# Kernel optimization log

Measured on AMD Instinct MI355X. Metric: run time of the kernel, lower is better.

Reference implementation:

```python
import jax, jax.numpy as jnp
import numpy as np

SIGMA = 1.0

def _pairwise_sqdist(x, y):
    # x: [N,3], y: [M,3] -> [N,M] squared distances via gram expansion
    xx = jnp.sum(x * x, axis=-1)[:, None]
    yy = jnp.sum(y * y, axis=-1)[None, :]
    xy = x @ y.T
    return jnp.maximum(xx + yy - 2.0 * xy, 0.0)

def _cauchy(d2, sigma):
    return 1.0 / (1.0 + d2 / (sigma * sigma))

def setup_inputs() -> dict:
    key = jax.random.key(0)
    k1, k2, k3, k4 = jax.random.split(key, 4)
    V, N, M = 4096, 8192, 8192
    src_vertices = jax.random.normal(k1, (V, 3), dtype=jnp.float32)
    tar_normals = jax.random.normal(k2, (M, 3), dtype=jnp.float32)
    tar_centers = jax.random.normal(k3, (M, 3), dtype=jnp.float32)
    src_indices = jax.random.randint(k4, (N, 3), 0, V)
    return {"src_vertices": src_vertices, "tar_normals": tar_normals,
            "tar_centers": tar_centers, "src_indices": src_indices}

def reference(src_vertices, tar_normals, tar_centers, src_indices):
    # Gather triangle vertices: [N,3(verts),3(xyz)]
    tris = src_vertices[src_indices]
    a, b, c = tris[:, 0, :], tris[:, 1, :], tris[:, 2, :]
    normals = 0.5 * jnp.cross(a - b, c - b)        # [N,3]
    centers = tris.sum(axis=1) / 3.0               # [N,3]

    # Currents energy with cauchy kernel K(x,y) = 1/(1 + |x-y|^2/sigma^2)
    K_ss = _cauchy(_pairwise_sqdist(centers, centers), SIGMA)      # [N,N]
    K_st = _cauchy(_pairwise_sqdist(centers, tar_centers), SIGMA)  # [N,M]
    K_tt = _cauchy(_pairwise_sqdist(tar_centers, tar_centers), SIGMA)  # [M,M]

    e_ss = jnp.sum(K_ss * (normals @ normals.T))
    e_st = jnp.sum(K_st * (normals @ tar_normals.T))
    e_tt = jnp.sum(K_tt * (tar_normals @ tar_normals.T))
    return e_ss - 2.0 * e_st + e_tt
```

## Files before the change

### kernel.cpp

```cpp
#include <hip/hip_runtime.h>

typedef short bf16x8 __attribute__((ext_vector_type(8)));
typedef float f32x16 __attribute__((ext_vector_type(16)));

static __device__ __forceinline__ unsigned short f2bf(float x) {
    unsigned u = __builtin_bit_cast(unsigned, x);
    unsigned r = (u + 0x7FFFu + ((u >> 16) & 1u)) >> 16;
    return (unsigned short)r;
}
static __device__ __forceinline__ float bf2f(unsigned short h) {
    unsigned u = (unsigned)h << 16;
    return __builtin_bit_cast(float, u);
}

__global__ void dc_pack(const float* __restrict__ verts,
                        const float* __restrict__ tnorm,
                        const float* __restrict__ tcent,
                        const int* __restrict__ idx,
                        unsigned short* __restrict__ ws,
                        float* __restrict__ out,
                        int N, int M) {
    int p = blockIdx.x * blockDim.x + threadIdx.x;
    if (p == 0) out[0] = 0.0f;
    int P = N + M;
    if (p >= P) return;

    float cx, cy, cz, nx, ny, nz;
    if (p < N) {
        int i0 = idx[3 * p + 0], i1 = idx[3 * p + 1], i2 = idx[3 * p + 2];
        float ax = verts[3 * i0], ay = verts[3 * i0 + 1], az = verts[3 * i0 + 2];
        float bx = verts[3 * i1], by = verts[3 * i1 + 1], bz = verts[3 * i1 + 2];
        float qx = verts[3 * i2], qy = verts[3 * i2 + 1], qz = verts[3 * i2 + 2];
        float ux = ax - bx, uy = ay - by, uz = az - bz;
        float vx = qx - bx, vy = qy - by, vz = qz - bz;
        nx = 0.5f * (uy * vz - uz * vy);
        ny = 0.5f * (uz * vx - ux * vz);
        nz = 0.5f * (ux * vy - uy * vx);
        cx = (ax + bx + qx) * (1.0f / 3.0f);
        cy = (ay + by + qy) * (1.0f / 3.0f);
        cz = (az + bz + qz) * (1.0f / 3.0f);
    } else {
        int t = p - N;
        cx = tcent[3 * t]; cy = tcent[3 * t + 1]; cz = tcent[3 * t + 2];
        nx = -tnorm[3 * t]; ny = -tnorm[3 * t + 1]; nz = -tnorm[3 * t + 2];
    }

    unsigned short chx = f2bf(cx), chy = f2bf(cy), chz = f2bf(cz);
    unsigned short clx = f2bf(cx - bf2f(chx));
    unsigned short cly = f2bf(cy - bf2f(chy));
    unsigned short clz = f2bf(cz - bf2f(chz));
    unsigned short nhx = f2bf(nx), nhy = f2bf(ny), nhz = f2bf(nz);
    unsigned short nlx = f2bf(nx - bf2f(nhx));
    unsigned short nly = f2bf(ny - bf2f(nhy));
    unsigned short nlz = f2bf(nz - bf2f(nhz));
    float ex = bf2f(chx) + bf2f(clx);
    float ey = bf2f(chy) + bf2f(cly);
    float ez = bf2f(chz) + bf2f(clz);
    float s = ex * ex + ey * ey + ez * ez;
    unsigned short sh = f2bf(s), sl = f2bf(s - bf2f(sh));
    unsigned short m2hx = f2bf(-2.0f * bf2f(chx)), m2hy = f2bf(-2.0f * bf2f(chy)), m2hz = f2bf(-2.0f * bf2f(chz));
    unsigned short m2lx = f2bf(-2.0f * bf2f(clx)), m2ly = f2bf(-2.0f * bf2f(cly)), m2lz = f2bf(-2.0f * bf2f(clz));
    const unsigned short one = 0x3F80;

    __align__(16) unsigned short A1v[16] = {
        m2hx, m2hy, m2hz,  m2hx, m2hy, m2hz,  m2lx, m2ly, m2lz,
        sh, sl,  one, one,  one,  0, 0 };
    __align__(16) unsigned short B1v[16] = {
        chx, chy, chz,  clx, cly, clz,  chx, chy, chz,
        one, one,  sh, sl,  one,  0, 0 };
    __align__(16) unsigned short A2v[16] = {
        nhx, nhy, nhz,  nhx, nhy, nhz,  nlx, nly, nlz,
        0, 0, 0, 0, 0, 0, 0 };
    __align__(16) unsigned short B2v[16] = {
        nhx, nhy, nhz,  nlx, nly, nlz,  nhx, nhy, nhz,
        0, 0, 0, 0, 0, 0, 0 };

    size_t arr = (size_t)P * 16;
    unsigned short* A1 = ws;
    unsigned short* B1 = ws + arr;
    unsigned short* A2 = ws + 2 * arr;
    unsigned short* B2 = ws + 3 * arr;

    int tile = p >> 5, m = p & 31;
    size_t lo = ((size_t)tile * 64 + m) * 8;
    size_t hi = lo + 32 * 8;

    *(uint4*)(A1 + lo) = *(const uint4*)&A1v[0];
    *(uint4*)(A1 + hi) = *(const uint4*)&A1v[8];
    *(uint4*)(B1 + lo) = *(const uint4*)&B1v[0];
    *(uint4*)(B1 + hi) = *(const uint4*)&B1v[8];
    *(uint4*)(A2 + lo) = *(const uint4*)&A2v[0];
    *(uint4*)(A2 + hi) = *(const uint4*)&A2v[8];
    *(uint4*)(B2 + lo) = *(const uint4*)&B2v[0];
    *(uint4*)(B2 + hi) = *(const uint4*)&B2v[8];
}

template <bool HALF>
static __device__ __forceinline__ void acc4(float4& part, const f32x16& d1, const f32x16& d2) {
#pragma unroll
    for (int g = 0; g < 4; ++g) {
        const int r = 4 * g;
        float p01 = d1[r] * d1[r + 1];
        float p23 = d1[r + 2] * d1[r + 3];
        float n01 = fmaf(d2[r], d1[r + 1], d2[r + 1] * d1[r]);
        float n23 = fmaf(d2[r + 2], d1[r + 3], d2[r + 3] * d1[r + 2]);
        float t   = p01 * p23;
        float num = fmaf(n01, p23, n23 * p01);
        float rk  = __builtin_amdgcn_rcpf(t);
        if (HALF) rk *= 0.5f;
        (&part.x)[g] = fmaf(num, rk, (&part.x)[g]);
    }
}

__global__ __launch_bounds__(256, 5) void dc_pair_mfma(
    const unsigned short* __restrict__ ws, float* __restrict__ out, int P) {
    __shared__ float wsum[4];

    const int nT = P >> 5;
    const int half = nT >> 1;
    size_t arr = (size_t)P * 16;
    const unsigned short* A1 = ws;
    const unsigned short* B1 = ws + arr;
    const unsigned short* A2 = ws + 2 * arr;
    const unsigned short* B2 = ws + 3 * arr;

    int tid = threadIdx.x;
    int lane = tid & 63, wv = tid >> 6;
    int g = blockIdx.x * 4 + wv;
    int I = g / 10;
    int c = g - 10 * I;

    int st  = c * 26 - (c > 7 ? c - 7 : 0);
    int len = 26 - (c >= 7 ? 1 : 0);

    bf16x8 a1 = *(const bf16x8*)(A1 + ((size_t)I * 64 + lane) * 8);
    bf16x8 a2 = *(const bf16x8*)(A2 + ((size_t)I * 64 + lane) * 8);

    const f32x16 zero = {0.f,0.f,0.f,0.f,0.f,0.f,0.f,0.f,0.f,0.f,0.f,0.f,0.f,0.f,0.f,0.f};
    float4 part = make_float4(0.f, 0.f, 0.f, 0.f);

#pragma unroll 2
    for (int it = 0; it < len; ++it) {
        int d = st + it;
        int j = I + d;
        int jm = (j >= nT) ? j - nT : j;
        const bf16x8 b1 = *(const bf16x8*)(B1 + ((size_t)jm * 64 + lane) * 8);
        const bf16x8 b2 = *(const bf16x8*)(B2 + ((size_t)jm * 64 + lane) * 8);
        f32x16 d1 = __builtin_amdgcn_mfma_f32_32x32x16_bf16(a1, b1, zero, 0, 0, 0);
        f32x16 d2 = __builtin_amdgcn_mfma_f32_32x32x16_bf16(a2, b2, zero, 0, 0, 0);
        if (d == 0 || d == half) acc4<true>(part, d1, d2);
        else                     acc4<false>(part, d1, d2);
    }

    float s = (part.x + part.y + part.z + part.w) * 2.0f;
#pragma unroll
    for (int off = 32; off > 0; off >>= 1) s += __shfl_down(s, off, 64);
    if (lane == 0) wsum[wv] = s;
    __syncthreads();
    if (tid == 0) {
        float t = wsum[0] + wsum[1] + wsum[2] + wsum[3];
        atomicAdd(out, t);
    }
}

extern "C" void kernel_launch(void* const* d_in, const int* in_sizes, int n_in,
                              void* d_out, int out_size, void* d_ws, size_t ws_size,
                              hipStream_t stream) {
    const float* verts = (const float*)d_in[0];
    const float* tnorm = (const float*)d_in[1];
    const float* tcent = (const float*)d_in[2];
    const int*   sidx  = (const int*)d_in[3];

    int M = in_sizes[1] / 3;
    int N = in_sizes[3] / 3;
    int P = N + M;

    unsigned short* ws = (unsigned short*)d_ws;
    float* out = (float*)d_out;

    int bblocks = (P + 255) / 256;
    dc_pack<<<bblocks, 256, 0, stream>>>(verts, tnorm, tcent, sidx, ws, out, N, M);

    int nT = P >> 5;
    int nBlocks = (nT * 10) / 4;
    dc_pair_mfma<<<nBlocks, 256, 0, stream>>>(ws, out, P);
}
```

Before: 90.42 us.

## Interleave B operands, prefetch next tile, and peel diagonal and half-diagonal tiles

Result: faster. 87.54 us (-3.2%).

```diff
diff --git a/kernel.cpp b/kernel.cpp
--- a/kernel.cpp
+++ b/kernel.cpp
@@ -12,6 +12,7 @@
     unsigned u = (unsigned)h << 16;
     return __builtin_bit_cast(float, u);
 }
+
 
 __global__ void dc_pack(const float* __restrict__ verts,
                         const float* __restrict__ tnorm,
@@ -77,9 +78,8 @@
 
     size_t arr = (size_t)P * 16;
     unsigned short* A1 = ws;
-    unsigned short* B1 = ws + arr;
-    unsigned short* A2 = ws + 2 * arr;
-    unsigned short* B2 = ws + 3 * arr;
+    unsigned short* A2 = ws + arr;
+    unsigned short* BB = ws + 2 * arr;
 
     int tile = p >> 5, m = p & 31;
     size_t lo = ((size_t)tile * 64 + m) * 8;
@@ -87,15 +87,17 @@
 
     *(uint4*)(A1 + lo) = *(const uint4*)&A1v[0];
     *(uint4*)(A1 + hi) = *(const uint4*)&A1v[8];
-    *(uint4*)(B1 + lo) = *(const uint4*)&B1v[0];
-    *(uint4*)(B1 + hi) = *(const uint4*)&B1v[8];
     *(uint4*)(A2 + lo) = *(const uint4*)&A2v[0];
     *(uint4*)(A2 + hi) = *(const uint4*)&A2v[8];
-    *(uint4*)(B2 + lo) = *(const uint4*)&B2v[0];
-    *(uint4*)(B2 + hi) = *(const uint4*)&B2v[8];
-}
-
-template <bool HALF>
+
+    size_t blo = ((size_t)tile * 64 + m) * 16;
+    size_t bhi = ((size_t)tile * 64 + 32 + m) * 16;
+    *(uint4*)(BB + blo)     = *(const uint4*)&B1v[0];
+    *(uint4*)(BB + blo + 8) = *(const uint4*)&B2v[0];
+    *(uint4*)(BB + bhi)     = *(const uint4*)&B1v[8];
+    *(uint4*)(BB + bhi + 8) = *(const uint4*)&B2v[8];
+}
+
 static __device__ __forceinline__ void acc4(float4& part, const f32x16& d1, const f32x16& d2) {
 #pragma unroll
     for (int g = 0; g < 4; ++g) {
@@ -106,9 +108,7 @@
         float n23 = fmaf(d2[r + 2], d1[r + 3], d2[r + 3] * d1[r + 2]);
         float t   = p01 * p23;
         float num = fmaf(n01, p23, n23 * p01);
-        float rk  = __builtin_amdgcn_rcpf(t);
-        if (HALF) rk *= 0.5f;
-        (&part.x)[g] = fmaf(num, rk, (&part.x)[g]);
+        (&part.x)[g] = fmaf(num, __builtin_amdgcn_rcpf(t), (&part.x)[g]);
     }
 }
 
@@ -117,12 +117,10 @@
     __shared__ float wsum[4];
 
     const int nT = P >> 5;
-    const int half = nT >> 1;
     size_t arr = (size_t)P * 16;
     const unsigned short* A1 = ws;
-    const unsigned short* B1 = ws + arr;
-    const unsigned short* A2 = ws + 2 * arr;
-    const unsigned short* B2 = ws + 3 * arr;
+    const unsigned short* A2 = ws + arr;
+    const unsigned short* BB = ws + 2 * arr;
 
     int tid = threadIdx.x;
     int lane = tid & 63, wv = tid >> 6;
@@ -132,27 +130,66 @@
 
     int st  = c * 26 - (c > 7 ? c - 7 : 0);
     int len = 26 - (c >= 7 ? 1 : 0);
+    int d0 = st, L = len, extra = 0, extraTile = 0;
+    if (c == 0) { d0 = 1; L = 25; extra = 1; extraTile = I; }
+    else if (c == 9) { L = 24; extra = 1;
+        extraTile = I + 256 - ((I + 256 >= nT) ? nT : 0); }
 
     bf16x8 a1 = *(const bf16x8*)(A1 + ((size_t)I * 64 + lane) * 8);
     bf16x8 a2 = *(const bf16x8*)(A2 + ((size_t)I * 64 + lane) * 8);
 
     const f32x16 zero = {0.f,0.f,0.f,0.f,0.f,0.f,0.f,0.f,0.f,0.f,0.f,0.f,0.f,0.f,0.f,0.f};
-    float4 part = make_float4(0.f, 0.f, 0.f, 0.f);
-
+    float4 partA = make_float4(0.f, 0.f, 0.f, 0.f);
+    float4 partB = make_float4(0.f, 0.f, 0.f, 0.f);
+
+    int js   = I + d0;
+    int len1 = nT - js; if (len1 > L) len1 = L; if (len1 < 0) len1 = 0;
+    int len2 = L - len1;
+    int startA = (len1 > 0) ? js : js - nT;
+
+    const size_t laneOff = (size_t)lane * 16;
+
+    {
+        const unsigned short* pb = BB + (size_t)startA * 1024 + laneOff;
+        bf16x8 b1 = *(const bf16x8*)pb;
+        bf16x8 b2 = *(const bf16x8*)(pb + 8);
 #pragma unroll 2
-    for (int it = 0; it < len; ++it) {
-        int d = st + it;
-        int j = I + d;
-        int jm = (j >= nT) ? j - nT : j;
-        const bf16x8 b1 = *(const bf16x8*)(B1 + ((size_t)jm * 64 + lane) * 8);
-        const bf16x8 b2 = *(const bf16x8*)(B2 + ((size_t)jm * 64 + lane) * 8);
+        for (int it = 0; it < len1; ++it) {
+            pb += 1024;
+            bf16x8 nb1 = *(const bf16x8*)pb;
+            bf16x8 nb2 = *(const bf16x8*)(pb + 8);
+            f32x16 d1 = __builtin_amdgcn_mfma_f32_32x32x16_bf16(a1, b1, zero, 0, 0, 0);
+            f32x16 d2 = __builtin_amdgcn_mfma_f32_32x32x16_bf16(a2, b2, zero, 0, 0, 0);
+            acc4(partA, d1, d2);
+            b1 = nb1; b2 = nb2;
+        }
+    }
+    if (len2 > 0) {
+        const unsigned short* pb = BB + (size_t)(js + len1 - nT) * 1024 + laneOff;
+        bf16x8 b1 = *(const bf16x8*)pb;
+        bf16x8 b2 = *(const bf16x8*)(pb + 8);
+#pragma unroll 2
+        for (int it = 0; it < len2; ++it) {
+            pb += 1024;
+            bf16x8 nb1 = *(const bf16x8*)pb;
+            bf16x8 nb2 = *(const bf16x8*)(pb + 8);
+            f32x16 d1 = __builtin_amdgcn_mfma_f32_32x32x16_bf16(a1, b1, zero, 0, 0, 0);
+            f32x16 d2 = __builtin_amdgcn_mfma_f32_32x32x16_bf16(a2, b2, zero, 0, 0, 0);
+            acc4(partA, d1, d2);
+            b1 = nb1; b2 = nb2;
+        }
+    }
+    for (int e = 0; e < extra; ++e) {
+        const unsigned short* pb = BB + (size_t)extraTile * 1024 + laneOff;
+        bf16x8 b1 = *(const bf16x8*)pb;
+        bf16x8 b2 = *(const bf16x8*)(pb + 8);
         f32x16 d1 = __builtin_amdgcn_mfma_f32_32x32x16_bf16(a1, b1, zero, 0, 0, 0);
         f32x16 d2 = __builtin_amdgcn_mfma_f32_32x32x16_bf16(a2, b2, zero, 0, 0, 0);
-        if (d == 0 || d == half) acc4<true>(part, d1, d2);
-        else                     acc4<false>(part, d1, d2);
-    }
-
-    float s = (part.x + part.y + part.z + part.w) * 2.0f;
+        acc4(partB, d1, d2);
+    }
+
+    float s = 2.0f * (partA.x + partA.y + partA.z + partA.w)
+            + (partB.x + partB.y + partB.z + partB.w);
 #pragma unroll
     for (int off = 32; off > 0; off >>= 1) s += __shfl_down(s, off, 64);
     if (lane == 0) wsum[wv] = s;
```

## Process two row tiles per wave to reuse B loads, software-prefetch B

Applied to the files above, without the earlier changes.

New measurement: 83.75 us. -7.4%, faster.

```diff
diff --git a/kernel.cpp b/kernel.cpp
--- a/kernel.cpp
+++ b/kernel.cpp
@@ -12,6 +12,7 @@
     unsigned u = (unsigned)h << 16;
     return __builtin_bit_cast(float, u);
 }
+
 
 __global__ void dc_pack(const float* __restrict__ verts,
                         const float* __restrict__ tnorm,
@@ -77,8 +78,8 @@
 
     size_t arr = (size_t)P * 16;
     unsigned short* A1 = ws;
-    unsigned short* B1 = ws + arr;
-    unsigned short* A2 = ws + 2 * arr;
+    unsigned short* A2 = ws + arr;
+    unsigned short* B1 = ws + 2 * arr;
     unsigned short* B2 = ws + 3 * arr;
 
     int tile = p >> 5, m = p & 31;
@@ -87,15 +88,14 @@
 
     *(uint4*)(A1 + lo) = *(const uint4*)&A1v[0];
     *(uint4*)(A1 + hi) = *(const uint4*)&A1v[8];
+    *(uint4*)(A2 + lo) = *(const uint4*)&A2v[0];
+    *(uint4*)(A2 + hi) = *(const uint4*)&A2v[8];
     *(uint4*)(B1 + lo) = *(const uint4*)&B1v[0];
     *(uint4*)(B1 + hi) = *(const uint4*)&B1v[8];
-    *(uint4*)(A2 + lo) = *(const uint4*)&A2v[0];
-    *(uint4*)(A2 + hi) = *(const uint4*)&A2v[8];
     *(uint4*)(B2 + lo) = *(const uint4*)&B2v[0];
     *(uint4*)(B2 + hi) = *(const uint4*)&B2v[8];
 }
 
-template <bool HALF>
 static __device__ __forceinline__ void acc4(float4& part, const f32x16& d1, const f32x16& d2) {
 #pragma unroll
     for (int g = 0; g < 4; ++g) {
@@ -106,53 +106,84 @@
         float n23 = fmaf(d2[r + 2], d1[r + 3], d2[r + 3] * d1[r + 2]);
         float t   = p01 * p23;
         float num = fmaf(n01, p23, n23 * p01);
-        float rk  = __builtin_amdgcn_rcpf(t);
-        if (HALF) rk *= 0.5f;
-        (&part.x)[g] = fmaf(num, rk, (&part.x)[g]);
-    }
-}
-
-__global__ __launch_bounds__(256, 5) void dc_pair_mfma(
+        (&part.x)[g] = fmaf(num, __builtin_amdgcn_rcpf(t), (&part.x)[g]);
+    }
+}
+
+__global__ __launch_bounds__(256, 4) void dc_pair_mfma(
     const unsigned short* __restrict__ ws, float* __restrict__ out, int P) {
     __shared__ float wsum[4];
 
     const int nT = P >> 5;
-    const int half = nT >> 1;
     size_t arr = (size_t)P * 16;
     const unsigned short* A1 = ws;
-    const unsigned short* B1 = ws + arr;
-    const unsigned short* A2 = ws + 2 * arr;
+    const unsigned short* A2 = ws + arr;
+    const unsigned short* B1 = ws + 2 * arr;
     const unsigned short* B2 = ws + 3 * arr;
 
     int tid = threadIdx.x;
     int lane = tid & 63, wv = tid >> 6;
-    int g = blockIdx.x * 4 + wv;
-    int I = g / 10;
-    int c = g - 10 * I;
-
-    int st  = c * 26 - (c > 7 ? c - 7 : 0);
-    int len = 26 - (c >= 7 ? 1 : 0);
-
-    bf16x8 a1 = *(const bf16x8*)(A1 + ((size_t)I * 64 + lane) * 8);
-    bf16x8 a2 = *(const bf16x8*)(A2 + ((size_t)I * 64 + lane) * 8);
+    int gi = blockIdx.x * 4 + wv;
+    int rp = gi >> 4, c = gi & 15;
+    int I0 = 2 * rp, I1 = I0 + 1;
+
+    const size_t lo = (size_t)lane * 8;
+
+    bf16x8 a1_0 = *(const bf16x8*)(A1 + (size_t)I0 * 512 + lo);
+    bf16x8 a2_0 = *(const bf16x8*)(A2 + (size_t)I0 * 512 + lo);
+    bf16x8 a1_1 = *(const bf16x8*)(A1 + (size_t)I1 * 512 + lo);
+    bf16x8 a2_1 = *(const bf16x8*)(A2 + (size_t)I1 * 512 + lo);
 
     const f32x16 zero = {0.f,0.f,0.f,0.f,0.f,0.f,0.f,0.f,0.f,0.f,0.f,0.f,0.f,0.f,0.f,0.f};
-    float4 part = make_float4(0.f, 0.f, 0.f, 0.f);
-
-#pragma unroll 2
-    for (int it = 0; it < len; ++it) {
-        int d = st + it;
-        int j = I + d;
-        int jm = (j >= nT) ? j - nT : j;
-        const bf16x8 b1 = *(const bf16x8*)(B1 + ((size_t)jm * 64 + lane) * 8);
-        const bf16x8 b2 = *(const bf16x8*)(B2 + ((size_t)jm * 64 + lane) * 8);
-        f32x16 d1 = __builtin_amdgcn_mfma_f32_32x32x16_bf16(a1, b1, zero, 0, 0, 0);
-        f32x16 d2 = __builtin_amdgcn_mfma_f32_32x32x16_bf16(a2, b2, zero, 0, 0, 0);
-        if (d == 0 || d == half) acc4<true>(part, d1, d2);
-        else                     acc4<false>(part, d1, d2);
-    }
-
-    float s = (part.x + part.y + part.z + part.w) * 2.0f;
+    float4 partA = make_float4(0.f, 0.f, 0.f, 0.f);
+    float4 corrP = make_float4(0.f, 0.f, 0.f, 0.f);
+    float4 corrM = make_float4(0.f, 0.f, 0.f, 0.f);
+
+    auto run = [&](int startTile, int n) {
+        const unsigned short* p1 = B1 + (size_t)startTile * 512 + lo;
+        const unsigned short* p2 = B2 + (size_t)startTile * 512 + lo;
+        bf16x8 b1 = *(const bf16x8*)p1;
+        bf16x8 b2 = *(const bf16x8*)p2;
+        for (int it = 0; it < n; ++it) {
+            p1 += 512; p2 += 512;
+            bf16x8 nb1 = *(const bf16x8*)p1;
+            bf16x8 nb2 = *(const bf16x8*)p2;
+            f32x16 d1 = __builtin_amdgcn_mfma_f32_32x32x16_bf16(a1_0, b1, zero, 0, 0, 0);
+            f32x16 d2 = __builtin_amdgcn_mfma_f32_32x32x16_bf16(a2_0, b2, zero, 0, 0, 0);
+            acc4(partA, d1, d2);
+            d1 = __builtin_amdgcn_mfma_f32_32x32x16_bf16(a1_1, b1, zero, 0, 0, 0);
+            d2 = __builtin_amdgcn_mfma_f32_32x32x16_bf16(a2_1, b2, zero, 0, 0, 0);
+            acc4(partA, d1, d2);
+            b1 = nb1; b2 = nb2;
+        }
+    };
+    auto one_tile = [&](float4& part, const bf16x8& x1, const bf16x8& x2, int jm) {
+        const bf16x8 b1 = *(const bf16x8*)(B1 + (size_t)jm * 512 + lo);
+        const bf16x8 b2 = *(const bf16x8*)(B2 + (size_t)jm * 512 + lo);
+        f32x16 d1 = __builtin_amdgcn_mfma_f32_32x32x16_bf16(x1, b1, zero, 0, 0, 0);
+        f32x16 d2 = __builtin_amdgcn_mfma_f32_32x32x16_bf16(x2, b2, zero, 0, 0, 0);
+        acc4(part, d1, d2);
+    };
+
+    int js = I0 + 1 + 16 * c;
+    int len1 = nT - js; if (len1 > 16) len1 = 16; if (len1 < 0) len1 = 0;
+    int len2 = 16 - len1;
+    if (len1 > 0) run(js, len1);
+    if (len2 > 0) run(js + len1 - nT, len2);
+
+    if (c == 0) {
+        one_tile(corrP, a1_0, a2_0, I0);
+        one_tile(corrM, a1_1, a2_1, I0 + 1);
+    } else if (c == 15) {
+        int v = I0 + 256; if (v >= nT) v -= nT;
+        int y = I0 + 257; if (y >= nT) y -= nT;
+        one_tile(corrM, a1_0, a2_0, v);
+        one_tile(corrP, a1_1, a2_1, y);
+    }
+
+    float s = 2.0f * (partA.x + partA.y + partA.z + partA.w)
+            + (corrP.x + corrP.y + corrP.z + corrP.w)
+            - (corrM.x + corrM.y + corrM.z + corrM.w);
 #pragma unroll
     for (int off = 32; off > 0; off >>= 1) s += __shfl_down(s, off, 64);
     if (lane == 0) wsum[wv] = s;
@@ -181,7 +212,5 @@
     int bblocks = (P + 255) / 256;
     dc_pack<<<bblocks, 256, 0, stream>>>(verts, tnorm, tcent, sidx, ws, out, N, M);
 
-    int nT = P >> 5;
-    int nBlocks = (nT * 10) / 4;
-    dc_pair_mfma<<<nBlocks, 256, 0, stream>>>(ws, out, P);
-}
+    dc_pair_mfma<<<1024, 256, 0, stream>>>(ws, out, P);
+}
```

## Re-partition the pair-tile loop into fixed 16-tile chunks with diagonal corrections

Applied to the files above, without the earlier changes.

After: 95.94 us. 1.06x slower.

```diff
diff --git a/kernel.cpp b/kernel.cpp
--- a/kernel.cpp
+++ b/kernel.cpp
@@ -12,6 +12,7 @@
     unsigned u = (unsigned)h << 16;
     return __builtin_bit_cast(float, u);
 }
+
 
 __global__ void dc_pack(const float* __restrict__ verts,
                         const float* __restrict__ tnorm,
@@ -77,8 +78,8 @@
 
     size_t arr = (size_t)P * 16;
     unsigned short* A1 = ws;
-    unsigned short* B1 = ws + arr;
-    unsigned short* A2 = ws + 2 * arr;
+    unsigned short* A2 = ws + arr;
+    unsigned short* B1 = ws + 2 * arr;
     unsigned short* B2 = ws + 3 * arr;
 
     int tile = p >> 5, m = p & 31;
@@ -87,15 +88,14 @@
 
     *(uint4*)(A1 + lo) = *(const uint4*)&A1v[0];
     *(uint4*)(A1 + hi) = *(const uint4*)&A1v[8];
+    *(uint4*)(A2 + lo) = *(const uint4*)&A2v[0];
+    *(uint4*)(A2 + hi) = *(const uint4*)&A2v[8];
     *(uint4*)(B1 + lo) = *(const uint4*)&B1v[0];
     *(uint4*)(B1 + hi) = *(const uint4*)&B1v[8];
-    *(uint4*)(A2 + lo) = *(const uint4*)&A2v[0];
-    *(uint4*)(A2 + hi) = *(const uint4*)&A2v[8];
     *(uint4*)(B2 + lo) = *(const uint4*)&B2v[0];
     *(uint4*)(B2 + hi) = *(const uint4*)&B2v[8];
 }
 
-template <bool HALF>
 static __device__ __forceinline__ void acc4(float4& part, const f32x16& d1, const f32x16& d2) {
 #pragma unroll
     for (int g = 0; g < 4; ++g) {
@@ -106,53 +106,63 @@
         float n23 = fmaf(d2[r + 2], d1[r + 3], d2[r + 3] * d1[r + 2]);
         float t   = p01 * p23;
         float num = fmaf(n01, p23, n23 * p01);
-        float rk  = __builtin_amdgcn_rcpf(t);
-        if (HALF) rk *= 0.5f;
-        (&part.x)[g] = fmaf(num, rk, (&part.x)[g]);
+        (&part.x)[g] = fmaf(num, __builtin_amdgcn_rcpf(t), (&part.x)[g]);
     }
 }
 
-__global__ __launch_bounds__(256, 5) void dc_pair_mfma(
+__global__ __launch_bounds__(256, 8) void dc_pair_mfma(
     const unsigned short* __restrict__ ws, float* __restrict__ out, int P) {
     __shared__ float wsum[4];
 
     const int nT = P >> 5;
-    const int half = nT >> 1;
     size_t arr = (size_t)P * 16;
     const unsigned short* A1 = ws;
-    const unsigned short* B1 = ws + arr;
-    const unsigned short* A2 = ws + 2 * arr;
+    const unsigned short* A2 = ws + arr;
+    const unsigned short* B1 = ws + 2 * arr;
     const unsigned short* B2 = ws + 3 * arr;
 
     int tid = threadIdx.x;
     int lane = tid & 63, wv = tid >> 6;
-    int g = blockIdx.x * 4 + wv;
-    int I = g / 10;
-    int c = g - 10 * I;
+    int gi = blockIdx.x * 4 + wv;
+    int I = gi >> 4, c = gi & 15;
 
-    int st  = c * 26 - (c > 7 ? c - 7 : 0);
-    int len = 26 - (c >= 7 ? 1 : 0);
+    const size_t lo = (size_t)lane * 8;
 
-    bf16x8 a1 = *(const bf16x8*)(A1 + ((size_t)I * 64 + lane) * 8);
-    bf16x8 a2 = *(const bf16x8*)(A2 + ((size_t)I * 64 + lane) * 8);
+    bf16x8 a1 = *(const bf16x8*)(A1 + (size_t)I * 512 + lo);
+    bf16x8 a2 = *(const bf16x8*)(A2 + (size_t)I * 512 + lo);
 
     const f32x16 zero = {0.f,0.f,0.f,0.f,0.f,0.f,0.f,0.f,0.f,0.f,0.f,0.f,0.f,0.f,0.f,0.f};
-    float4 part = make_float4(0.f, 0.f, 0.f, 0.f);
+    float4 partA = make_float4(0.f, 0.f, 0.f, 0.f);
 
-#pragma unroll 2
-    for (int it = 0; it < len; ++it) {
-        int d = st + it;
-        int j = I + d;
-        int jm = (j >= nT) ? j - nT : j;
-        const bf16x8 b1 = *(const bf16x8*)(B1 + ((size_t)jm * 64 + lane) * 8);
-        const bf16x8 b2 = *(const bf16x8*)(B2 + ((size_t)jm * 64 + lane) * 8);
+    int js = I + 1 + 16 * c;
+#pragma unroll 1
+    for (int it = 0; it < 16; ++it) {
+        int j = js + it; if (j >= nT) j -= nT;
+        size_t o = (size_t)j * 512 + lo;
+        bf16x8 b1 = *(const bf16x8*)(B1 + o);
+        bf16x8 b2 = *(const bf16x8*)(B2 + o);
         f32x16 d1 = __builtin_amdgcn_mfma_f32_32x32x16_bf16(a1, b1, zero, 0, 0, 0);
         f32x16 d2 = __builtin_amdgcn_mfma_f32_32x32x16_bf16(a2, b2, zero, 0, 0, 0);
-        if (d == 0 || d == half) acc4<true>(part, d1, d2);
-        else                     acc4<false>(part, d1, d2);
+        acc4(partA, d1, d2);
     }
 
-    float s = (part.x + part.y + part.z + part.w) * 2.0f;
+    float s = 2.0f * (partA.x + partA.y + partA.z + partA.w);
+
+    if (c == 0 || c == 15) {
+        int jm;
+        if (c == 0) jm = I;
+        else { jm = I + 256; if (jm >= nT) jm -= nT; }
+        size_t o = (size_t)jm * 512 + lo;
+        bf16x8 b1 = *(const bf16x8*)(B1 + o);
+        bf16x8 b2 = *(const bf16x8*)(B2 + o);
+        f32x16 d1 = __builtin_amdgcn_mfma_f32_32x32x16_bf16(a1, b1, zero, 0, 0, 0);
+        f32x16 d2 = __builtin_amdgcn_mfma_f32_32x32x16_bf16(a2, b2, zero, 0, 0, 0);
+        float4 corr = make_float4(0.f, 0.f, 0.f, 0.f);
+        acc4(corr, d1, d2);
+        float cs = corr.x + corr.y + corr.z + corr.w;
+        s += (c == 0) ? cs : -cs;
+    }
+
 #pragma unroll
     for (int off = 32; off > 0; off >>= 1) s += __shfl_down(s, off, 64);
     if (lane == 0) wsum[wv] = s;
@@ -181,7 +191,5 @@
     int bblocks = (P + 255) / 256;
     dc_pack<<<bblocks, 256, 0, stream>>>(verts, tnorm, tcent, sidx, ws, out, N, M);
 
-    int nT = P >> 5;
-    int nBlocks = (nT * 10) / 4;
-    dc_pair_mfma<<<nBlocks, 256, 0, stream>>>(ws, out, P);
+    dc_pair_mfma<<<2048, 256, 0, stream>>>(ws, out, P);
 }
```
